# Performance work log

Hardware: AMD Instinct MI355X
Metric: run time of the kernel (lower is better)

The kernel has to match this reference:

```python
import jax, jax.numpy as jnp
import numpy as np

DIM = 1024
HEADS = 16
HD = DIM // HEADS          # 64
HID = 4 * DIM              # 4096
TPF = 1374                 # tokens_per_frame
LR = 0.1
NS_ITERS = 5
TTT_STEPS = 2
B, S = 2, 4
SN = S * TPF               # 5496


def _newton_schulz(G, iters=NS_ITERS):
    """Muon Newton-Schulz orthogonalization (quintic iteration)."""
    a, b, c = 3.4445, -4.7750, 2.0315
    X = G / (jnp.linalg.norm(G) + 1e-7)
    transposed = G.shape[0] > G.shape[1]
    if transposed:
        X = X.T
    for _ in range(iters):
        A = X @ X.T                      # [m,m], m = min(rows, cols)
        X = a * X + (b * A + c * (A @ A)) @ X
    return X.T if transposed else X


def _muon_update(p, g):
    return p - LR * _newton_schulz(g)


def setup_inputs() -> dict:
    key = jax.random.key(0)
    ks = jax.random.split(key, 8)
    inp = {
        "x": jax.random.normal(ks[0], (B, SN, DIM), jnp.float32),
        "qkv_w": jax.random.normal(ks[1], (DIM, 3 * DIM), jnp.float32) * (DIM ** -0.5),
        "qkv_b": jnp.zeros((3 * DIM,), jnp.float32),
        "qn_scale": jnp.ones((HD,), jnp.float32),
        "qn_bias": jnp.zeros((HD,), jnp.float32),
        "kn_scale": jnp.ones((HD,), jnp.float32),
        "kn_bias": jnp.zeros((HD,), jnp.float32),
        # theta: lecun-normal scale (std = 1/sqrt(fan_in))
        "ttt_gate": jax.random.normal(ks[2], (DIM, HID), jnp.float32) * (DIM ** -0.5),
        "ttt_val": jax.random.normal(ks[3], (DIM, HID), jnp.float32) * (DIM ** -0.5),
        "ttt_proj": jax.random.normal(ks[4], (HID, DIM), jnp.float32) * (HID ** -0.5),
        "proj_w": jax.random.normal(ks[5], (DIM, DIM), jnp.float32) * (DIM ** -0.5),
        "proj_b": jnp.zeros((DIM,), jnp.float32),
    }
    return inp


def reference(x, qkv_w, qkv_b, qn_scale, qn_bias, kn_scale, kn_bias,
              ttt_gate, ttt_val, ttt_proj, proj_w, proj_b):
    Bx, SNx, _ = x.shape
    qkv = x @ qkv_w + qkv_b                       # [B, SN, 3*DIM]
    q, k, v = jnp.split(qkv, 3, axis=-1)
    q = q.reshape(Bx, SNx, HEADS, HD)
    k = k.reshape(Bx, SNx, HEADS, HD)
    # per-head L2 normalize then affine NormLayer (x*scale + bias)
    q = q / (jnp.linalg.norm(q, axis=-1, keepdims=True) + 1e-6) * qn_scale + qn_bias
    k = k / (jnp.linalg.norm(k, axis=-1, keepdims=True) + 1e-6) * kn_scale + kn_bias
    q_ttt = q.reshape(-1, DIM)                    # [B*SN, DIM]
    k_ttt = k.reshape(-1, DIM)
    # no short_conv param at init -> v_mixed is identity, so v_target == v
    v_ttt = v.reshape(-1, DIM)

    theta = {"gate": ttt_gate, "val": ttt_val, "proj": ttt_proj}

    def loss_fn(p):
        h = jax.nn.swish(k_ttt @ p["gate"]) * (k_ttt @ p["val"])   # [B*SN, HID]
        pred = h @ p["proj"]                                        # [B*SN, DIM]
        return jnp.mean((pred - v_ttt) ** 2)

    for _ in range(TTT_STEPS):
        grads = jax.grad(loss_fn)(theta)
        theta = {kk: _muon_update(theta[kk], grads[kk]) for kk in theta}

    h_q = jax.nn.swish(q_ttt @ theta["gate"]) * (q_ttt @ theta["val"])
    o = (h_q @ theta["proj"]) @ proj_w + proj_b
    return o.reshape(Bx, SNx, DIM)
```

## Files before the change

### kernel.cpp

```cpp
#include <hip/hip_runtime.h>
#include <stdint.h>

#define NTOK 10992
#define NTOKA 11264
#define PMi 4194304

typedef unsigned short u16;
typedef __attribute__((ext_vector_type(8))) __bf16 b8;
typedef __attribute__((ext_vector_type(4))) float f32x4;

__device__ __forceinline__ u16 f2b(float f) {
  union { float f; uint32_t u; } v; v.f = f;
  return (u16)((v.u + 0x7fffu + ((v.u >> 16) & 1u)) >> 16);
}
__device__ __forceinline__ float b2f(u16 b) {
  union { uint32_t u; float f; } v; v.u = ((uint32_t)b) << 16; return v.f;
}
__device__ __forceinline__ uint2 pk4(u16 a, u16 b, u16 c, u16 d) {
  uint2 r; r.x = (uint32_t)a | ((uint32_t)b << 16); r.y = (uint32_t)c | ((uint32_t)d << 16);
  return r;
}
__device__ __forceinline__ void gload16(const u16* g, u16* l) {
  __builtin_amdgcn_global_load_lds((const __attribute__((address_space(1))) void*)(const void*)g,
                                   (__attribute__((address_space(3))) void*)(void*)l, 16, 0, 0);
}

struct GA {
  const u16* A[3]; const u16* B[3];
  void* C[3]; u16* O1[3]; u16* OT[3];
  const void* E0[3]; const u16* E1[3];
  int lda[3], ldb[3];
  int M, N, K, ldc, ldo1, ldt, lde0, lde1;
  float p0, p1;
};

template <int EPI, int SPLIT>
__global__ __launch_bounds__(256, 2) void gemm_bt(GA g) {
  __shared__ u16 As[128 * 32];
  __shared__ u16 Bs[128 * 32];
  int bz = blockIdx.z, koff = 0, klen = g.K;
  if constexpr (SPLIT) { koff = (bz & 1) * (g.K >> 1); bz >>= 1; klen = g.K >> 1; }
  const u16* __restrict__ A = g.A[bz] + koff;
  const u16* __restrict__ B = g.B[bz] + koff;
  const int lda = g.lda[bz], ldb = g.ldb[bz];
  const int m0 = blockIdx.y * 128, n0 = blockIdx.x * 128;
  const int tid = threadIdx.x, w = tid >> 6, lane = tid & 63;
  const int wr = (w >> 1) * 64, wc = (w & 1) * 64;
  const int ln = lane & 15, lq = lane >> 4;

  f32x4 acc[4][4];
#pragma unroll
  for (int i = 0; i < 4; ++i)
#pragma unroll
    for (int j = 0; j < 4; ++j)
#pragma unroll
      for (int r = 0; r < 4; ++r) acc[i][j][r] = 0.f;

  const u16* Ag = A + (size_t)(m0 + 32 * w + (lane >> 2)) * lda + (lane & 3) * 8;
  const u16* Bg = B + (size_t)(n0 + 32 * w + (lane >> 2)) * ldb + (lane & 3) * 8;
  u16* AsW = &As[w * 1024];
  u16* BsW = &Bs[w * 1024];
  const int nkt = klen >> 5;

  for (int kt = 0; kt < nkt; ++kt) {
    __syncthreads();
    gload16(Ag, AsW);
    gload16(Ag + (size_t)16 * lda, AsW + 512);
    gload16(Bg, BsW);
    gload16(Bg + (size_t)16 * ldb, BsW + 512);
    Ag += 32; Bg += 32;
    __syncthreads();
    b8 af[4], bfr[4];
#pragma unroll
    for (int i = 0; i < 4; ++i) af[i] = *(const b8*)&As[(wr + i * 16 + ln) * 32 + lq * 8];
#pragma unroll
    for (int j = 0; j < 4; ++j) bfr[j] = *(const b8*)&Bs[(wc + j * 16 + ln) * 32 + lq * 8];
#pragma unroll
    for (int i = 0; i < 4; ++i)
#pragma unroll
      for (int j = 0; j < 4; ++j)
        acc[i][j] = __builtin_amdgcn_mfma_f32_16x16x32_bf16(af[i], bfr[j], acc[i][j], 0, 0, 0);
  }

  float* Cf = (float*)g.C[bz];
  u16* Cb = (u16*)g.C[bz];
  u16* O1 = g.O1[bz];
  const float* E0f = (const float*)g.E0[bz];
  const u16* E0b = (const u16*)g.E0[bz];
  const u16* E1b = g.E1[bz];

#pragma unroll
  for (int i = 0; i < 4; ++i) {
    const int mb = m0 + wr + i * 16 + lq * 4;
    if (mb >= g.M) continue;
#pragma unroll
    for (int j = 0; j < 4; ++j) {
      const int n = n0 + wc + j * 16 + ln;
      if (n >= g.N) continue;
      float vv[4];
#pragma unroll
      for (int r = 0; r < 4; ++r) vv[r] = acc[i][j][r];
      if constexpr (EPI == 0) {
#pragma unroll
        for (int r = 0; r < 4; ++r) Cb[(size_t)(mb + r) * g.ldc + n] = f2b(vv[r]);
      } else if constexpr (EPI == 1) {
        const float bias = E0f[n];
#pragma unroll
        for (int r = 0; r < 4; ++r) Cb[(size_t)(mb + r) * g.ldc + n] = f2b(vv[r] + bias);
      } else if constexpr (EPI == 5) {
        u16 cq[4], oq[4];
#pragma unroll
        for (int r = 0; r < 4; ++r) {
          const int m = mb + r;
          const float f1 = b2f(E0b[(size_t)m * g.lde0 + n]);
          const float f2 = b2f(E1b[(size_t)m * g.lde1 + n]);
          cq[r] = f2b(vv[r] * f1);
          oq[r] = f2b(vv[r] * f2);
        }
        *(uint2*)&Cb[(size_t)n * g.ldt + mb] = pk4(cq[0], cq[1], cq[2], cq[3]);
        *(uint2*)&O1[(size_t)n * g.ldt + mb] = pk4(oq[0], oq[1], oq[2], oq[3]);
      } else if constexpr (EPI == 6) {
        const float bias = E0f[n];
#pragma unroll
        for (int r = 0; r < 4; ++r) Cf[(size_t)(mb + r) * g.ldc + n] = vv[r] + bias;
      } else if constexpr (EPI == 8) {
#pragma unroll
        for (int r = 0; r < 4; ++r) atomicAdd(&Cf[(size_t)(mb + r) * g.ldc + n], vv[r]);
      } else if constexpr (EPI == 16) {
        uint2 old = *(const uint2*)&Cb[(size_t)n * 1024 + mb];
        u16 nq[4];
        nq[0] = f2b(b2f((u16)(old.x & 0xffff)) - 0.1f * vv[0]);
        nq[1] = f2b(b2f((u16)(old.x >> 16)) - 0.1f * vv[1]);
        nq[2] = f2b(b2f((u16)(old.y & 0xffff)) - 0.1f * vv[2]);
        nq[3] = f2b(b2f((u16)(old.y >> 16)) - 0.1f * vv[3]);
        *(uint2*)&Cb[(size_t)n * 1024 + mb] = pk4(nq[0], nq[1], nq[2], nq[3]);
        if (O1) {
#pragma unroll
          for (int r = 0; r < 4; ++r) O1[(size_t)(mb + r) * 4096 + n] = nq[r];
        }
      }
    }
  }
}

__global__ __launch_bounds__(256, 2) void gemm_qkv(GA g) {
  __shared__ u16 As[128 * 32];
  __shared__ u16 Bs[128 * 32];
  const u16* __restrict__ A = g.A[0];
  const u16* __restrict__ B = g.B[0];
  const int lda = g.lda[0], ldb = g.ldb[0];
  const int m0 = blockIdx.y * 128, n0 = blockIdx.x * 128;
  const int tid = threadIdx.x, w = tid >> 6, lane = tid & 63;
  const int wr = (w >> 1) * 64, wc = (w & 1) * 64;
  const int ln = lane & 15, lq = lane >> 4;

  f32x4 acc[4][4];
#pragma unroll
  for (int i = 0; i < 4; ++i)
#pragma unroll
    for (int j = 0; j < 4; ++j)
#pragma unroll
      for (int r = 0; r < 4; ++r) acc[i][j][r] = 0.f;

  const u16* Ag = A + (size_t)(m0 + 32 * w + (lane >> 2)) * lda + (lane & 3) * 8;
  const u16* Bg = B + (size_t)(n0 + 32 * w + (lane >> 2)) * ldb + (lane & 3) * 8;
  u16* AsW = &As[w * 1024];
  u16* BsW = &Bs[w * 1024];
  const int nkt = g.K >> 5;

  for (int kt = 0; kt < nkt; ++kt) {
    __syncthreads();
    gload16(Ag, AsW);
    gload16(Ag + (size_t)16 * lda, AsW + 512);
    gload16(Bg, BsW);
    gload16(Bg + (size_t)16 * ldb, BsW + 512);
    Ag += 32; Bg += 32;
    __syncthreads();
    b8 af[4], bfr[4];
#pragma unroll
    for (int i = 0; i < 4; ++i) af[i] = *(const b8*)&As[(wr + i * 16 + ln) * 32 + lq * 8];
#pragma unroll
    for (int j = 0; j < 4; ++j) bfr[j] = *(const b8*)&Bs[(wc + j * 16 + ln) * 32 + lq * 8];
#pragma unroll
    for (int i = 0; i < 4; ++i)
#pragma unroll
      for (int j = 0; j < 4; ++j)
        acc[i][j] = __builtin_amdgcn_mfma_f32_16x16x32_bf16(af[i], bfr[j], acc[i][j], 0, 0, 0);
  }

  u16* qbp = (u16*)g.C[0];
  u16* kbp = g.O1[0];
  u16* kTp = g.OT[0];
  u16* vTp = g.OT[1];
  const float* bias = (const float*)g.E0[0];
  const float* qS = (const float*)g.E0[1];
  const float* kS = (const float*)g.E0[2];
  const float* qB = (const float*)g.E1[0];
  const float* kB = (const float*)g.E1[1];
  const int seg = (n0 + wc) >> 10;

#pragma unroll
  for (int i = 0; i < 4; ++i) {
    const int mb = m0 + wr + i * 16 + lq * 4;
    if (mb >= g.M) continue;
    float vb4[4][4];
// ... 378 lines not shown
#pragma unroll
        for (int r = 0; r < 4; ++r) acc[i][j][r] = 0.f;
    const u16* Ag = A + (size_t)(m0 + 32 * w + (lane >> 2)) * lda + (lane & 3) * 8;
    const u16* Bg = B + (size_t)(n0 + 32 * w + (lane >> 2)) * ldb + (lane & 3) * 8;
    u16* AsW = &As[w * 1024];
    u16* BsW = &Bs[w * 1024];
    const int nkt = gdh.K >> 5;
    for (int kt = 0; kt < nkt; ++kt) {
      __syncthreads();
      gload16(Ag, AsW);
      gload16(Ag + (size_t)16 * lda, AsW + 512);
      gload16(Bg, BsW);
      gload16(Bg + (size_t)16 * ldb, BsW + 512);
      Ag += 32; Bg += 32;
      __syncthreads();
      b8 af[4], bfr[4];
#pragma unroll
      for (int i = 0; i < 4; ++i) af[i] = *(const b8*)&As[(wr + i * 16 + ln) * 32 + lq * 8];
#pragma unroll
      for (int j = 0; j < 4; ++j) bfr[j] = *(const b8*)&Bs[(wc + j * 16 + ln) * 32 + lq * 8];
#pragma unroll
      for (int i = 0; i < 4; ++i)
#pragma unroll
        for (int j = 0; j < 4; ++j)
          acc[i][j] = __builtin_amdgcn_mfma_f32_16x16x32_bf16(af[i], bfr[j], acc[i][j], 0, 0, 0);
    }
    u16* Cb = (u16*)gdh.C[0];
    u16* O1 = gdh.O1[0];
    const u16* E0b = (const u16*)gdh.E0[0];
    const u16* E1b = gdh.E1[0];
#pragma unroll
    for (int i = 0; i < 4; ++i) {
      const int mb = m0 + wr + i * 16 + lq * 4;
      if (mb >= gdh.M) continue;
#pragma unroll
      for (int j = 0; j < 4; ++j) {
        const int n = n0 + wc + j * 16 + ln;
        u16 cq[4], oq[4];
#pragma unroll
        for (int r = 0; r < 4; ++r) {
          const int m = mb + r;
          const float f1 = b2f(E0b[(size_t)m * gdh.lde0 + n]);
          const float f2 = b2f(E1b[(size_t)m * gdh.lde1 + n]);
          cq[r] = f2b(acc[i][j][r] * f1);
          oq[r] = f2b(acc[i][j][r] * f2);
        }
        *(uint2*)&Cb[(size_t)n * gdh.ldt + mb] = pk4(cq[0], cq[1], cq[2], cq[3]);
        *(uint2*)&O1[(size_t)n * gdh.ldt + mb] = pk4(oq[0], oq[1], oq[2], oq[3]);
      }
    }
  }
}

__global__ __launch_bounds__(256, 2) void fused_gd(GA ggr, GA gdp, int nGr, int dpx) {
  __shared__ u16 As[128 * 32];
  __shared__ u16 Bs[128 * 32];
  const int tid = threadIdx.x, w = tid >> 6, lane = tid & 63;
  const int ln = lane & 15, lq = lane >> 4;
  const int bid = blockIdx.x;

  if (bid < nGr) {
    const int wr = (w >> 1) * 64, wc = (w & 1) * 64;
    const int n0 = (bid & 31) * 128;
    const int rest = bid >> 5;
    const int m0 = (rest & 7) * 128;
    int bz = rest >> 3;
    const int koff = (bz & 1) * (ggr.K >> 1); bz >>= 1;
    const int klen = ggr.K >> 1;
    const u16* __restrict__ A = ggr.A[bz] + koff;
    const u16* __restrict__ B = ggr.B[bz] + koff;
    const int lda = ggr.lda[bz], ldb = ggr.ldb[bz];
    f32x4 acc[4][4];
#pragma unroll
    for (int i = 0; i < 4; ++i)
#pragma unroll
      for (int j = 0; j < 4; ++j)
#pragma unroll
        for (int r = 0; r < 4; ++r) acc[i][j][r] = 0.f;
    const u16* Ag = A + (size_t)(m0 + 32 * w + (lane >> 2)) * lda + (lane & 3) * 8;
    const u16* Bg = B + (size_t)(n0 + 32 * w + (lane >> 2)) * ldb + (lane & 3) * 8;
    u16* AsW = &As[w * 1024];
    u16* BsW = &Bs[w * 1024];
    const int nkt = klen >> 5;
    for (int kt = 0; kt < nkt; ++kt) {
      __syncthreads();
      gload16(Ag, AsW);
      gload16(Ag + (size_t)16 * lda, AsW + 512);
      gload16(Bg, BsW);
      gload16(Bg + (size_t)16 * ldb, BsW + 512);
      Ag += 32; Bg += 32;
      __syncthreads();
      b8 af[4], bfr[4];
#pragma unroll
      for (int i = 0; i < 4; ++i) af[i] = *(const b8*)&As[(wr + i * 16 + ln) * 32 + lq * 8];
#pragma unroll
      for (int j = 0; j < 4; ++j) bfr[j] = *(const b8*)&Bs[(wc + j * 16 + ln) * 32 + lq * 8];
#pragma unroll
      for (int i = 0; i < 4; ++i)
#pragma unroll
        for (int j = 0; j < 4; ++j)
          acc[i][j] = __builtin_amdgcn_mfma_f32_16x16x32_bf16(af[i], bfr[j], acc[i][j], 0, 0, 0);
    }
    float* Cf = (float*)ggr.C[bz];
#pragma unroll
    for (int i = 0; i < 4; ++i) {
      const int mb = m0 + wr + i * 16 + lq * 4;
#pragma unroll
      for (int j = 0; j < 4; ++j) {
        const int n = n0 + wc + j * 16 + ln;
#pragma unroll
        for (int r = 0; r < 4; ++r) atomicAdd(&Cf[(size_t)(mb + r) * ggr.ldc + n], acc[i][j][r]);
      }
    }
  } else {
    const int wr = (w >> 1) * 32, wc = (w & 1) * 32;
    const int l = bid - nGr;
    const int n0 = (l % dpx) * 64;
    const int m0 = (l / dpx) * 64;
    const u16* __restrict__ A = gdp.A[0];
    const u16* __restrict__ B = gdp.B[0];
    const int lda = gdp.lda[0], ldb = gdp.ldb[0];
    f32x4 acc[2][2];
#pragma unroll
    for (int i = 0; i < 2; ++i)
#pragma unroll
      for (int j = 0; j < 2; ++j)
#pragma unroll
        for (int r = 0; r < 4; ++r) acc[i][j][r] = 0.f;
    const u16* Ag = A + (size_t)(m0 + 16 * w + (lane >> 2)) * lda + (lane & 3) * 8;
    const u16* Bg = B + (size_t)(n0 + 16 * w + (lane >> 2)) * ldb + (lane & 3) * 8;
    u16* AsW = &As[w * 512];
    u16* BsW = &Bs[w * 512];
    const int nkt = gdp.K >> 5;
    for (int kt = 0; kt < nkt; ++kt) {
      __syncthreads();
      gload16(Ag, AsW);
      gload16(Bg, BsW);
      Ag += 32; Bg += 32;
      __syncthreads();
      b8 af[2], bfr[2];
#pragma unroll
      for (int i = 0; i < 2; ++i) af[i] = *(const b8*)&As[(wr + i * 16 + ln) * 32 + lq * 8];
#pragma unroll
      for (int j = 0; j < 2; ++j) bfr[j] = *(const b8*)&Bs[(wc + j * 16 + ln) * 32 + lq * 8];
#pragma unroll
      for (int i = 0; i < 2; ++i)
#pragma unroll
        for (int j = 0; j < 2; ++j)
          acc[i][j] = __builtin_amdgcn_mfma_f32_16x16x32_bf16(af[i], bfr[j], acc[i][j], 0, 0, 0);
    }
    u16* Cb = (u16*)gdp.C[0];
    u16* OT = gdp.OT[0];
    const u16* E0b = (const u16*)gdp.E0[0];
#pragma unroll
    for (int i = 0; i < 2; ++i) {
      const int mb = m0 + wr + i * 16 + lq * 4;
#pragma unroll
      for (int j = 0; j < 2; ++j) {
        const int n = n0 + wc + j * 16 + ln;
        if (n >= gdp.N) continue;
        u16 cq[4];
#pragma unroll
        for (int r = 0; r < 4; ++r) {
          const int m = mb + r;
// ... 147 lines not shown
    }
  } else {
    const int m0 = ((int)blockIdx.y - ysplit) * 128, n0 = blockIdx.x * 128;
    const u16* __restrict__ A = gp.A[0];
    const u16* __restrict__ B = gp.B[0];
    const int lda = gp.lda[0], ldb = gp.ldb[0];
    f32x4 acc[4][4];
#pragma unroll
    for (int i = 0; i < 4; ++i)
#pragma unroll
      for (int j = 0; j < 4; ++j)
#pragma unroll
        for (int r = 0; r < 4; ++r) acc[i][j][r] = 0.f;
    const u16* Ag = A + (size_t)(m0 + 32 * w + (lane >> 2)) * lda + (lane & 3) * 8;
    const u16* Bg = B + (size_t)(n0 + 32 * w + (lane >> 2)) * ldb + (lane & 3) * 8;
    u16* AsW = &As[w * 1024];
    u16* BsW = &Bs[w * 1024];
    const int nkt = gp.K >> 5;
    for (int kt = 0; kt < nkt; ++kt) {
      __syncthreads();
      gload16(Ag, AsW);
      gload16(Ag + (size_t)16 * lda, AsW + 512);
      gload16(Bg, BsW);
      gload16(Bg + (size_t)16 * ldb, BsW + 512);
      Ag += 32; Bg += 32;
      __syncthreads();
      b8 af[4], bfr[4];
#pragma unroll
      for (int i = 0; i < 4; ++i) af[i] = *(const b8*)&As[(wr + i * 16 + ln) * 32 + lq * 8];
#pragma unroll
      for (int j = 0; j < 4; ++j) bfr[j] = *(const b8*)&Bs[(wc + j * 16 + ln) * 32 + lq * 8];
#pragma unroll
      for (int i = 0; i < 4; ++i)
#pragma unroll
        for (int j = 0; j < 4; ++j)
          acc[i][j] = __builtin_amdgcn_mfma_f32_16x16x32_bf16(af[i], bfr[j], acc[i][j], 0, 0, 0);
    }
    u16* Cb = (u16*)gp.C[0];
#pragma unroll
    for (int i = 0; i < 4; ++i) {
      const int mb = m0 + wr + i * 16 + lq * 4;
#pragma unroll
      for (int j = 0; j < 4; ++j) {
        const int n = n0 + wc + j * 16 + ln;
#pragma unroll
        for (int r = 0; r < 4; ++r) Cb[(size_t)(mb + r) * gp.ldc + n] = f2b(acc[i][j][r]);
      }
    }
  }
}

template <int EPI>
__global__ __launch_bounds__(256, 2) void gemm64(GA g) {
  if constexpr (EPI == 10 || EPI == 11 || EPI == 12) {
    if (blockIdx.x > blockIdx.y) return;
  }
  __shared__ u16 As[64 * 32];
  __shared__ u16 Bs[64 * 32];
  const int bz = blockIdx.z;
  const u16* __restrict__ A = g.A[bz];
  const u16* __restrict__ B = g.B[bz];
  const int lda = g.lda[bz], ldb = g.ldb[bz];
  const int m0 = blockIdx.y * 64, n0 = blockIdx.x * 64;
  const int tid = threadIdx.x, w = tid >> 6, lane = tid & 63;
  const int wr = (w >> 1) * 32, wc = (w & 1) * 32;
  const int ln = lane & 15, lq = lane >> 4;

  f32x4 acc[2][2];
#pragma unroll
  for (int i = 0; i < 2; ++i)
#pragma unroll
    for (int j = 0; j < 2; ++j)
#pragma unroll
      for (int r = 0; r < 4; ++r) acc[i][j][r] = 0.f;

  const u16* Ag = A + (size_t)(m0 + 16 * w + (lane >> 2)) * lda + (lane & 3) * 8;
  const u16* Bg = B + (size_t)(n0 + 16 * w + (lane >> 2)) * ldb + (lane & 3) * 8;
  u16* AsW = &As[w * 512];
  u16* BsW = &Bs[w * 512];
  const int nkt = g.K >> 5;

  for (int kt = 0; kt < nkt; ++kt) {
    __syncthreads();
    gload16(Ag, AsW);
    gload16(Bg, BsW);
    Ag += 32; Bg += 32;
    __syncthreads();
    b8 af[2], bfr[2];
#pragma unroll
    for (int i = 0; i < 2; ++i) af[i] = *(const b8*)&As[(wr + i * 16 + ln) * 32 + lq * 8];
#pragma unroll
    for (int j = 0; j < 2; ++j) bfr[j] = *(const b8*)&Bs[(wc + j * 16 + ln) * 32 + lq * 8];
#pragma unroll
    for (int i = 0; i < 2; ++i)
#pragma unroll
      for (int j = 0; j < 2; ++j)
        acc[i][j] = __builtin_amdgcn_mfma_f32_16x16x32_bf16(af[i], bfr[j], acc[i][j], 0, 0, 0);
  }

  u16* Cb = (u16*)g.C[bz];
  u16* OT = g.OT[bz];
  const u16* E0b = (const u16*)g.E0[bz];
  const u16* E1b = g.E1[bz];
  const bool offdiag = (blockIdx.x != blockIdx.y);

#pragma unroll
  for (int i = 0; i < 2; ++i) {
// ... 2 lines not shown
#pragma unroll
    for (int j = 0; j < 2; ++j) {
      const int n = n0 + wc + j * 16 + ln;
      if (n >= g.N) continue;
      float vv[4];
#pragma unroll
      for (int r = 0; r < 4; ++r) vv[r] = acc[i][j][r];
      if constexpr (EPI == 0) {
#pragma unroll
        for (int r = 0; r < 4; ++r) Cb[(size_t)(mb + r) * g.ldc + n] = f2b(vv[r]);
      } else if constexpr (EPI == 2) {
        u16 cq[4];
#pragma unroll
        for (int r = 0; r < 4; ++r) {
          const int m = mb + r;
          const u16 ub = f2b((vv[r] - b2f(E0b[(size_t)m * g.lde0 + n])) * g.p0);
          Cb[(size_t)m * g.ldc + n] = ub;
          cq[r] = ub;
        }
        *(uint2*)&OT[(size_t)n * g.ldt + mb] = pk4(cq[0], cq[1], cq[2], cq[3]);
      } else if constexpr (EPI == 10) {
        u16 cq[4];
#pragma unroll
        for (int r = 0; r < 4; ++r) {
          cq[r] = f2b(vv[r]);
          Cb[(size_t)(mb + r) * g.ldc + n] = cq[r];
        }
        if (offdiag)
          *(uint2*)&Cb[(size_t)n * g.ldc + mb] = pk4(cq[0], cq[1], cq[2], cq[3]);
      } else if constexpr (EPI == 11) {
        u16 cq[4];
#pragma unroll
        for (int r = 0; r < 4; ++r) {
          cq[r] = f2b(g.p0 * b2f(E0b[(size_t)(mb + r) * g.lde0 + n]) + g.p1 * vv[r]);
          Cb[(size_t)(mb + r) * g.ldc + n] = cq[r];
        }
        if (offdiag)
          *(uint2*)&Cb[(size_t)n * g.ldc + mb] = pk4(cq[0], cq[1], cq[2], cq[3]);
      } else if constexpr (EPI == 12) {
        const uint2 t2u = *(const uint2*)&E1b[(size_t)n * g.lde1 + mb];
        const float t2v[4] = { b2f((u16)(t2u.x & 0xffff)), b2f((u16)(t2u.x >> 16)),
                               b2f((u16)(t2u.y & 0xffff)), b2f((u16)(t2u.y >> 16)) };
        u16 cq[4];
#pragma unroll
        for (int r = 0; r < 4; ++r) {
          const int m = mb + r;
          const float t1 = b2f(E1b[(size_t)m * g.lde1 + n]);
          const float a0 = b2f(E0b[(size_t)m * g.lde0 + n]);
          cq[r] = f2b(g.p0 * a0 + g.p1 * (t1 + t2v[r]) + vv[r]);
          Cb[(size_t)m * g.ldc + n] = cq[r];
        }
        if (offdiag)
          *(uint2*)&Cb[(size_t)n * g.ldc + mb] = pk4(cq[0], cq[1], cq[2], cq[3]);
      } else if constexpr (EPI == 15) {
        const uint2 eu = *(const uint2*)&E0b[(size_t)n * g.lde0 + mb];
        const float e4[4] = { b2f((u16)(eu.x & 0xffff)), b2f((u16)(eu.x >> 16)),
                              b2f((u16)(eu.y & 0xffff)), b2f((u16)(eu.y >> 16)) };
#pragma unroll
        for (int r = 0; r < 4; ++r)
          Cb[(size_t)(mb + r) * g.ldc + n] = f2b(g.p0 * e4[r] + vv[r]);
      }
    }
  }
}

__global__ __launch_bounds__(256) void tr_f32b(const float* __restrict__ in, u16* __restrict__ out,
                                               int Cin, int Rtot) {
  __shared__ u16 t[32][33];
  const int c0 = blockIdx.x * 32, r0 = blockIdx.y * 32;
  const int tx = threadIdx.x, ty = threadIdx.y;
#pragma unroll
  for (int yy = 0; yy < 4; ++yy) {
    const int rr = ty * 4 + yy;
    t[rr][tx] = f2b(in[(size_t)(r0 + rr) * Cin + c0 + tx]);
  }
  __syncthreads();
#pragma unroll
  for (int yy = 0; yy < 4; ++yy) {
    const int cc = ty * 4 + yy;
    out[(size_t)(c0 + cc) * Rtot + r0 + tx] = t[tx][cc];
  }
}

__global__ void cvt_k(const float* __restrict__ in, u16* __restrict__ out, int n) {
  const int i = blockIdx.x * 256 + threadIdx.x;
  if (i < n) out[i] = f2b(in[i]);
}

__global__ void diag_k(float* __restrict__ out, int n, float val) {
  const int i = blockIdx.x * 256 + threadIdx.x;
  if (i < n) out[i] = val;
}

__global__ void addI_k(const u16* __restrict__ W, u16* __restrict__ M, float a) {
  const int i = blockIdx.x * 256 + threadIdx.x;
  const size_t o = (size_t)blockIdx.y * 1048576;
  u16 v = W[o + i];
  if ((i >> 10) == (i & 1023)) v = f2b(a + b2f(v));
  M[o + i] = v;
}

__global__ __launch_bounds__(256) void sumsq_k(const float* __restrict__ g, float* __restrict__ out) {
  const int b = blockIdx.y;
  const float* p = g + (size_t)b * PMi;
  float s = 0.f;
  for (int i = blockIdx.x * 256 + threadIdx.x; i < PMi; i += gridDim.x * 256) {
    float v = p[i]; s += v * v;
  }
  for (int off = 32; off > 0; off >>= 1) s += __shfl_xor(s, off);
  __shared__ float red[4];
  if ((threadIdx.x & 63) == 0) red[threadIdx.x >> 6] = s;
  __syncthreads();
  if (threadIdx.x == 0) atomicAdd(out + b, red[0] + red[1] + red[2] + red[3]);
}

__global__ __launch_bounds__(256) void scale_tr(const float* __restrict__ g, const float* __restrict__ ss,
                                                u16* __restrict__ Xb, u16* __restrict__ XbT) {
  const int b = blockIdx.z;
  __shared__ u16 t[32][33];
  const float r = 1.f / (sqrtf(ss[b]) + 1e-7f);
  const float* G = g + (size_t)b * PMi;
  u16* X = Xb + (size_t)b * PMi;
  u16* XT = XbT + (size_t)b * PMi;
  const int j0 = blockIdx.x * 32, i0 = blockIdx.y * 32;
  const int tx = threadIdx.x, ty = threadIdx.y;
#pragma unroll
  for (int yy = 0; yy < 4; ++yy) {
    const int rr = ty * 4 + yy;
    const u16 v = f2b(G[(size_t)(i0 + rr) * 4096 + j0 + tx] * r);
    X[(size_t)(i0 + rr) * 4096 + j0 + tx] = v;
    t[rr][tx] = v;
  }
  __syncthreads();
#pragma unroll
  for (int yy = 0; yy < 4; ++yy) {
    const int cc = ty * 4 + yy;
    XT[(size_t)(j0 + cc) * 1024 + i0 + tx] = t[tx][cc];
  }
}

static GA mk(const u16* A, const u16* B, void* C, int M, int N, int K,
             int lda, int ldb, int ldc) {
  GA a{};
  a.A[0] = a.A[1] = a.A[2] = A;
  a.B[0] = a.B[1] = a.B[2] = B;
  a.C[0] = a.C[1] = a.C[2] = C;
  a.lda[0] = a.lda[1] = a.lda[2] = lda;
  a.ldb[0] = a.ldb[1] = a.ldb[2] = ldb;
  a.M = M; a.N = N; a.K = K; a.ldc = ldc;
  return a;
}

extern "C" void kernel_launch(void* const* d_in, const int* in_sizes, int n_in,
                              void* d_out, int out_size, void* d_ws, size_t ws_size,
                              hipStream_t stream) {
  (void)in_sizes; (void)n_in;
  const float* x      = (const float*)d_in[0];
  const float* qkv_w  = (const float*)d_in[1];
  const float* qkv_b  = (const float*)d_in[2];
  const float* qn_s   = (const float*)d_in[3];
  const float* qn_b   = (const float*)d_in[4];
  const float* kn_s   = (const float*)d_in[5];
  const float* kn_b   = (const float*)d_in[6];
  const float* g_gate = (const float*)d_in[7];
  const float* g_val  = (const float*)d_in[8];
  const float* g_proj = (const float*)d_in[9];
  const float* proj_w = (const float*)d_in[10];
  const float* proj_b = (const float*)d_in[11];
  float* out = (float*)d_out;

  const size_t PM = PMi;
  const size_t TD = (size_t)NTOKA * 1024;
  const size_t PERS = 127926528ull;

  auto needD = [&](int chk) {
    return PERS + 9ull * (size_t)chk * 8192 + 4ull * (size_t)chk * 2048 + 50331648ull + 8192;
  };
  auto needP = [&](int chk) {
    return PERS + 7ull * (size_t)chk * 8192 + 2ull * (size_t)chk * 2048 + 50331648ull + 8192;
  };
  auto needU = [&](int chk) {
    return PERS + 5ull * (size_t)chk * 8192 + 2ull * (size_t)chk * 2048 + 50331648ull + 4096;
  };
  int CHKr, MODE;
  if      (ws_size >= needD(5632)) { CHKr = 5632; MODE = 2; }
  else if (ws_size >= needD(4096)) { CHKr = 4096; MODE = 2; }
  else if (ws_size >= needP(5632)) { CHKr = 5632; MODE = 1; }
  else if (ws_size >= needU(5632)) { CHKr = 5632; MODE = 0; }
  else if (ws_size >= needP(2816)) { CHKr = 2816; MODE = 1; }
  else if (ws_size >= needP(2048)) { CHKr = 2048; MODE = 1; }
  else if (ws_size >= needU(1408)) { CHKr = 1408; MODE = 0; }
  else {
    diag_k<<<dim3((out_size + 255) / 256), dim3(256), 0, stream>>>(out, out_size,
                                                                   (float)(ws_size >> 20));
    return;
  }

  char* p = (char*)d_ws;
  auto carve = [&](size_t bytes) { char* r = p; p += (bytes + 255) & ~(size_t)255; return (void*)r; };
  auto cdiv = [](int a, int b) { return (a + b - 1) / b; };

  u16* Gt     = (u16*)carve(PM * 2);
  u16* Vt     = (u16*)carve(PM * 2);
  u16* Pt     = (u16*)carve(PM * 2);
  u16* Pb     = (u16*)carve(PM * 2);
  u16* projWt = (u16*)carve(1048576ull * 2);
  u16* qb     = (u16*)carve(TD * 2);
  u16* kb     = (u16*)carve(TD * 2);
  u16* vT     = (u16*)carve(TD * 2);
  u16* kT     = (u16*)carve(TD * 2);
  float* ssq  = (float*)carve(256);
  char* arena = p;

  u16* xb    = (u16*)arena;
  u16* qkvWt = (u16*)(arena + 23068672);
  const size_t CB = (size_t)CHKr * 4096 * 2;
  const size_t DP = (size_t)CHKr * 1024 * 2;
  u16 *f1A[2], *f2A[2], *hhA[2], *hTA[2], *dpTA[2], *dpBA[2], *dzvT;
  float* gAll;
  if (MODE == 2) {
    f1A[0] = (u16*)(arena + 0 * CB);  f2A[0] = (u16*)(arena + 1 * CB);
    hhA[0] = (u16*)(arena + 2 * CB);  hTA[0] = (u16*)(arena + 3 * CB);
    f1A[1] = (u16*)(arena + 4 * CB);  f2A[1] = (u16*)(arena + 5 * CB);
    hhA[1] = (u16*)(arena + 6 * CB);  hTA[1] = (u16*)(arena + 7 * CB);
    dzvT   = (u16*)(arena + 8 * CB);
    dpTA[0] = (u16*)(arena + 9 * CB);          dpBA[0] = (u16*)(arena + 9 * CB + DP);
    dpTA[1] = (u16*)(arena + 9 * CB + 2 * DP); dpBA[1] = (u16*)(arena + 9 * CB + 3 * DP);
    gAll = (float*)(arena + 9 * CB + 4 * DP);
  } else {
    f1A[0] = f1A[1] = (u16*)arena;
    f2A[0] = f2A[1] = (u16*)(arena + CB);
    hhA[0] = (u16*)(arena + 2 * CB);
    hTA[0] = (u16*)(arena + 3 * CB);
    dzvT   = (u16*)(arena + 4 * CB);
    dpTA[0] = dpTA[1] = (u16*)(arena + 5 * CB);
    dpBA[0] = dpBA[1] = (u16*)(arena + 5 * CB + DP);
    gAll = (float*)(arena + 5 * CB + 2 * DP);
    hhA[1] = (MODE == 1) ? (u16*)(arena + 5 * CB + 2 * DP + 3 * PM * 4) : hhA[0];
    hTA[1] = (MODE == 1) ? (u16*)(arena + 6 * CB + 2 * DP + 3 * PM * 4) : hTA[0];
  }
  u16* XAb  = (u16*)arena;
  u16* XAbT = (u16*)(arena + 25165824);
  u16* Ab   = (u16*)(arena + 50331648);
  u16* Wb   = (u16*)(arena + 56623104);
  u16* Tb   = (u16*)(arena + 62914560);
  u16* Mb0  = (u16*)(arena + 69206016);
  u16* Mb1  = (u16*)(arena + 75497472);
  u16* hbuf = (u16*)arena;
  u16* PWt  = (u16*)(arena + 92274688);

  const dim3 blk(256), tb32(32, 8);
  const float inv2 = 2.0f / (10992.0f * 1024.0f);
  const float nsa = 3.4445f, nsb = -4.7750f, nsc = 2.0315f;

  hipMemsetAsync(kT, 0, TD * 2, stream);
  hipMemsetAsync(vT, 0, TD * 2, stream);
  cvt_k<<<dim3(43968), blk, 0, stream>>>(x, xb, NTOK * 1024);
  cvt_k<<<dim3(16384), blk, 0, stream>>>(g_proj, Pb, (int)PM);
  tr_f32b<<<dim3(96, 32), tb32, 0, stream>>>(qkv_w, qkvWt, 3072, 1024);
  tr_f32b<<<dim3(32, 32), tb32, 0, stream>>>(proj_w, projWt, 1024, 1024);
  tr_f32b<<<dim3(128, 32), tb32, 0, stream>>>(g_gate, Gt, 4096, 1024);
  tr_f32b<<<dim3(128, 32), tb32, 0, stream>>>(g_val, Vt, 4096, 1024);
  tr_f32b<<<dim3(32, 128), tb32, 0, stream>>>(g_proj, Pt, 1024, 4096);

  {
    GA a = mk(xb, qkvWt, qb, NTOK, 3072, 1024, 1024, 1024, 1024);
    a.O1[0] = kb; a.OT[0] = kT; a.OT[1] = vT;
    a.E0[0] = qkv_b; a.E0[1] = qn_s; a.E0[2] = kn_s;
    a.E1[0] = (const u16*)qn_b; a.E1[1] = (const u16*)kn_b;
    gemm_qkv<<<dim3(24, 86, 1), blk, 0, stream>>>(a);
  }

  for (int step = 0; step < 2; ++step) {
    hipMemsetAsync(gAll, 0, 3 * PM * 4, stream);
    if (MODE == 2) {
      const int NC = cdiv(NTOK, CHKr);
      int c0P = 0, vcP = 0, mtP = 0;
      for (int ci = 0; ci < NC; ++ci) {
        const int c0 = ci * CHKr;
        const int vc = (NTOK - c0 < CHKr) ? (NTOK - c0) : CHKr;
        const int mt = cdiv(vc, 128);
        const int par = ci & 1, parP = par ^ 1;
        const int tail = (ci == NC - 1 && vc < CHKr);
        if (tail) hipMemsetAsync(hTA[par], 0, CB, stream);
        GA agv{};
        agv.A[0] = kb + (size_t)c0 * 1024; agv.lda[0] = 1024;
        agv.B[0] = Gt; agv.B[1] = Vt; agv.ldb[0] = 1024;
        agv.C[0] = f1A[par]; agv.O1[0] = f2A[par]; agv.O1[1] = hhA[par]; agv.OT[0] = hTA[par];
        agv.M = vc; agv.N = 4096; agv.K = 1024; agv.ldc = 4096; agv.ldt = CHKr;
        if (ci == 0) {
          gemm_gv<0><<<dim3(32, mt, 1), blk, 0, stream>>>(agv);
        } else {
          GA adh{};
          adh.A[0] = dpBA[parP]; adh.B[0] = Pb; adh.lda[0] = 1024; adh.ldb[0] = 1024;
          adh.C[0] = hhA[parP]; adh.O1[0] = dzvT;
          adh.E0[0] = f1A[parP]; adh.E1[0] = f2A[parP];
          adh.M = vcP; adh.N = 4096; adh.K = 1024; adh.ldt = CHKr;
          adh.lde0 = 4096; adh.lde1 = 4096;
          fused_hg<<<dim3(32, mt + mtP, 1), blk, 0, stream>>>(adh, agv, mt);
        }
        if (tail) hipMemsetAsync(dpTA[par], 0, DP, stream);
        GA adp = mk(Pt, hhA[par], dpTA[par], 1024, vc, 4096, 4096, 4096, CHKr);
        adp.OT[0] = dpBA[par]; adp.ldt = 1024;
        adp.E0[0] = vT + c0; adp.lde0 = NTOKA; adp.p0 = inv2;
        const int dpx = cdiv(vc, 64);
        if (ci == 0) {
          gemm64<2><<<dim3(dpx, 16, 1), blk, 0, stream>>>(adp);
        } else {
          GA agr{};
          agr.A[0] = kT + c0P; agr.A[1] = kT + c0P; agr.A[2] = dpTA[parP];
          agr.lda[0] = NTOKA; agr.lda[1] = NTOKA; agr.lda[2] = CHKr;
          agr.B[0] = hhA[parP]; agr.B[1] = dzvT; agr.B[2] = hTA[parP];
          agr.ldb[0] = agr.ldb[1] = agr.ldb[2] = CHKr;
          agr.C[0] = gAll; agr.C[1] = gAll + PM; agr.C[2] = gAll + 2 * PM;
          agr.M = 1024; agr.N = 4096; agr.K = CHKr; agr.ldc = 4096;
          fused_gd<<<dim3(1536 + dpx * 16, 1, 1), blk, 0, stream>>>(agr, adp, 1536, dpx);
        }
        c0P = c0; vcP = vc; mtP = mt;
      }
      const int par = (NC - 1) & 1;
      if (vcP < CHKr) {
        hipMemsetAsync(hhA[par], 0, CB, stream);
        hipMemsetAsync(dzvT, 0, CB, stream);
      }
      {
        GA adh = mk(dpBA[par], Pb, hhA[par], vcP, 4096, 1024, 1024, 1024, 0);
        adh.O1[0] = dzvT; adh.ldt = CHKr;
        adh.E0[0] = f1A[par]; adh.lde0 = 4096; adh.E1[0] = f2A[par]; adh.lde1 = 4096;
        gemm_bt<5, 0><<<dim3(32, mtP, 1), blk, 0, stream>>>(adh);
      }
      {
        GA agr{};
        agr.A[0] = kT + c0P; agr.A[1] = kT + c0P; agr.A[2] = dpTA[par];
        agr.lda[0] = NTOKA; agr.lda[1] = NTOKA; agr.lda[2] = CHKr;
        agr.B[0] = hhA[par]; agr.B[1] = dzvT; agr.B[2] = hTA[par];
        agr.ldb[0] = agr.ldb[1] = agr.ldb[2] = CHKr;
        agr.C[0] = gAll; agr.C[1] = gAll + PM; agr.C[2] = gAll + 2 * PM;
        agr.M = 1024; agr.N = 4096; agr.K = CHKr; agr.ldc = 4096;
        gemm_bt<8, 1><<<dim3(32, 8, 6), blk, 0, stream>>>(agr);
      }
    } else {
      int havePend = 0;
      GA pendGA{};
      for (int ci = 0, c0 = 0; c0 < NTOK; ++ci, c0 += CHKr) {
        const int vc = (NTOK - c0 < CHKr) ? (NTOK - c0) : CHKr;
        const int mt = cdiv(vc, 128);
        const u16* kc = kb + (size_t)c0 * 1024;
        u16* hhp = hhA[ci & 1];
        u16* hTp = hTA[ci & 1];
        if (vc < CHKr) hipMemsetAsync(hTp, 0, CB, stream);
        {
          GA agv{};
          agv.A[0] = kc; agv.lda[0] = 1024;
          agv.B[0] = Gt; agv.B[1] = Vt; agv.ldb[0] = 1024;
          agv.C[0] = f1A[0]; agv.O1[0] = f2A[0]; agv.O1[1] = hhp; agv.OT[0] = hTp;
          agv.M = vc; agv.N = 4096; agv.K = 1024; agv.ldc = 4096; agv.ldt = CHKr;
          if (MODE == 1 && havePend) {
            fused_gg<<<dim3(32, mt + 48, 1), blk, 0, stream>>>(pendGA, agv, mt);
            havePend = 0;
          } else {
            gemm_gv<0><<<dim3(32, mt, 1), blk, 0, stream>>>(agv);
          }
        }
        if (vc < CHKr) {
          hipMemsetAsync(dzvT, 0, CB, stream);
          hipMemsetAsync(dpTA[0], 0, DP, stream);
        }
        {
          GA a = mk(Pt, hhp, dpTA[0], 1024, vc, 4096, 4096, 4096, CHKr);
          a.OT[0] = dpBA[0]; a.ldt = 1024;
          a.E0[0] = vT + c0; a.lde0 = NTOKA; a.p0 = inv2;
          gemm64<2><<<dim3(cdiv(vc, 64), 16, 1), blk, 0, stream>>>(a);
        }
        if (vc < CHKr) hipMemsetAsync(hhp, 0, CB, stream);
        {
          GA a = mk(dpBA[0], Pb, hhp, vc, 4096, 1024, 1024, 1024, 0);
          a.O1[0] = dzvT; a.ldt = CHKr;
          a.E0[0] = f1A[0]; a.lde0 = 4096; a.E1[0] = f2A[0]; a.lde1 = 4096;
          gemm_bt<5, 0><<<dim3(32, mt, 1), blk, 0, stream>>>(a);
        }
        {
          GA a{};
          a.A[0] = kT + c0; a.A[1] = kT + c0; a.A[2] = dpTA[0];
          a.lda[0] = NTOKA; a.lda[1] = NTOKA; a.lda[2] = CHKr;
          a.B[0] = hhp; a.B[1] = dzvT; a.B[2] = hTp;
          a.ldb[0] = a.ldb[1] = a.ldb[2] = CHKr;
          a.C[0] = gAll; a.C[1] = gAll + PM; a.C[2] = gAll + 2 * PM;
          a.M = 1024; a.N = 4096; a.K = CHKr; a.ldc = 4096;
          const int last = (c0 + CHKr >= NTOK);
          if (MODE == 1 && !last) { pendGA = a; havePend = 1; }
          else gemm_bt<8, 1><<<dim3(32, 8, 6), blk, 0, stream>>>(a);
        }
      }
    }
    hipMemsetAsync(ssq, 0, 16, stream);
    sumsq_k<<<dim3(512, 3), blk, 0, stream>>>(gAll, ssq);
    scale_tr<<<dim3(128, 32, 3), tb32, 0, stream>>>(gAll, ssq, XAb, XAbT);

    {
      GA a{};
      for (int b = 0; b < 3; ++b) {
        a.A[b] = XAb + (size_t)b * PM; a.B[b] = XAb + (size_t)b * PM;
        a.C[b] = Ab + (size_t)b * 1048576;
        a.lda[b] = 4096; a.ldb[b] = 4096;
      }
      a.M = 1024; a.N = 1024; a.K = 4096; a.ldc = 1024;
      gemm64<10><<<dim3(16, 16, 3), blk, 0, stream>>>(a);
    }
    for (int it = 0; it < 5; ++it) {
      {
        GA a{};
        for (int b = 0; b < 3; ++b) {
          a.A[b] = Ab + (size_t)b * 1048576; a.B[b] = Ab + (size_t)b * 1048576;
          a.C[b] = Wb + (size_t)b * 1048576; a.E0[b] = Ab + (size_t)b * 1048576;
          a.lda[b] = 1024; a.ldb[b] = 1024;
        }
        a.M = 1024; a.N = 1024; a.K = 1024; a.ldc = 1024; a.lde0 = 1024;
        a.p0 = nsb; a.p1 = nsc;
        gemm64<11><<<dim3(16, 16, 3), blk, 0, stream>>>(a);
      }
      if (it == 0) {
        addI_k<<<dim3(4096, 3), blk, 0, stream>>>(Wb, Mb0, nsa);
        {
          GA a{};
          for (int b = 0; b < 3; ++b) {
            a.A[b] = Wb + (size_t)b * 1048576; a.B[b] = Ab + (size_t)b * 1048576;
            a.C[b] = Tb + (size_t)b * 1048576;
            a.lda[b] = 1024; a.ldb[b] = 1024;
          }
          a.M = 1024; a.N = 1024; a.K = 1024; a.ldc = 1024;
          gemm64<0><<<dim3(16, 16, 3), blk, 0, stream>>>(a);
        }
      } else if (it < 4) {
        u16* Mti = (it & 1) ? Mb0 : Mb1;
        u16* Mto = (it & 1) ? Mb1 : Mb0;
        GA gt{}, gm{};
        for (int b = 0; b < 3; ++b) {
          gt.A[b] = Wb + (size_t)b * 1048576; gt.B[b] = Ab + (size_t)b * 1048576;
          gt.C[b] = Tb + (size_t)b * 1048576;
          gt.lda[b] = 1024; gt.ldb[b] = 1024;
          gm.A[b] = Mti + (size_t)b * 1048576; gm.B[b] = Wb + (size_t)b * 1048576;
          gm.C[b] = Mto + (size_t)b * 1048576; gm.E0[b] = Mti + (size_t)b * 1048576;
          gm.lda[b] = 1024; gm.ldb[b] = 1024;
        }
        gt.M = gt.N = 1024; gt.K = 1024; gt.ldc = 1024;
        gm.M = gm.N = 1024; gm.K = 1024; gm.ldc = 1024; gm.lde0 = 1024; gm.p0 = nsa;
        fused_mt<<<dim3(16, 32, 3), blk, 0, stream>>>(gt, gm);
      } else {
        GA a{};
        for (int b = 0; b < 3; ++b) {
          a.A[b] = Wb + (size_t)b * 1048576; a.B[b] = Mb1 + (size_t)b * 1048576;
          a.C[b] = Mb0 + (size_t)b * 1048576; a.E0[b] = Mb1 + (size_t)b * 1048576;
          a.lda[b] = 1024; a.ldb[b] = 1024;
        }
        a.M = 1024; a.N = 1024; a.K = 1024; a.ldc = 1024; a.lde0 = 1024; a.p0 = nsa;
        gemm64<15><<<dim3(16, 16, 3), blk, 0, stream>>>(a);
      }
      if (it < 4) {
        GA a{};
        for (int b = 0; b < 3; ++b) {
          a.A[b] = Tb + (size_t)b * 1048576; a.B[b] = Wb + (size_t)b * 1048576;
          a.C[b] = Ab + (size_t)b * 1048576;
          a.E0[b] = Ab + (size_t)b * 1048576; a.E1[b] = Tb + (size_t)b * 1048576;
          a.lda[b] = 1024; a.ldb[b] = 1024;
        }
        a.M = 1024; a.N = 1024; a.K = 1024; a.ldc = 1024;
        a.lde0 = 1024; a.lde1 = 1024;
        a.p0 = nsa * nsa; a.p1 = nsa;
        gemm64<12><<<dim3(16, 16, 3), blk, 0, stream>>>(a);
      }
    }
    {
      GA a{};
      for (int b = 0; b < 3; ++b) {
        a.A[b] = Mb0 + (size_t)b * 1048576; a.B[b] = XAbT + (size_t)b * PM;
// ... 25 lines not shown
```

Measured before the change: 5.569 ms.

## Fuse setup transposes into QKV GEMM, drop memsets and addI kernel

Folds the weight conversions and transposes (gate, val, proj, proj_w and the bf16 copy of proj) into extra blocks of the QKV GEMM launch, so they share one kernel. It replaces the full-buffer memsets of kT/vT with a tail-zeroing kernel and fuses the Newton-Schulz identity add into a new GEMM epilogue. The gradient GEMM drops split-K in MODE 2, with the first chunk storing instead of atomically adding, which removes the gAll memset. It also clips the final chunk's K to skip padding. These changes cut launch count and memory traffic, but they rely on the tail zeroing and the first-chunk store covering every element that was previously cleared.

Result: no change. 5.648 ms (+1.4%).

```diff
diff --git a/kernel.cpp b/kernel.cpp
--- a/kernel.cpp
+++ b/kernel.cpp
@@ -32,6 +32,11 @@
   int lda[3], ldb[3];
   int M, N, K, ldc, ldo1, ldt, lde0, lde1;
   float p0, p1;
+};
+
+struct SP {
+  const float *gg, *gv, *gp, *pw;
+  u16 *Gt, *Vt, *Pt, *projWt, *Pb;
 };
 
 template <int EPI, int SPLIT>
@@ -103,10 +108,6 @@
       if constexpr (EPI == 0) {
 #pragma unroll
         for (int r = 0; r < 4; ++r) Cb[(size_t)(mb + r) * g.ldc + n] = f2b(vv[r]);
-      } else if constexpr (EPI == 1) {
-        const float bias = E0f[n];
-#pragma unroll
-        for (int r = 0; r < 4; ++r) Cb[(size_t)(mb + r) * g.ldc + n] = f2b(vv[r] + bias);
       } else if constexpr (EPI == 5) {
         u16 cq[4], oq[4];
 #pragma unroll
@@ -143,14 +144,47 @@
   }
 }
 
-__global__ __launch_bounds__(256, 2) void gemm_qkv(GA g) {
+__global__ __launch_bounds__(256, 2) void setup_fused(GA g, SP s) {
   __shared__ u16 As[128 * 32];
   __shared__ u16 Bs[128 * 32];
+  const int tid = threadIdx.x;
+
+  if ((int)blockIdx.y >= 86) {
+    const int id = ((int)blockIdx.y - 86) * 24 + (int)blockIdx.x;
+    if (id >= 14336) return;
+    if (id >= 13312) {
+      const int off = (id - 13312) * 4096;
+#pragma unroll 4
+      for (int i = tid; i < 4096; i += 256) s.Pb[off + i] = f2b(s.gp[off + i]);
+      return;
+    }
+    const float* in; u16* outp; int Cin, Rtot, bx, by;
+    if (id < 4096)       { in = s.gg; outp = s.Gt; Cin = 4096; Rtot = 1024; bx = id & 127; by = id >> 7; }
+    else if (id < 8192)  { const int t2 = id - 4096; in = s.gv; outp = s.Vt; Cin = 4096; Rtot = 1024; bx = t2 & 127; by = t2 >> 7; }
+    else if (id < 12288) { const int t2 = id - 8192; in = s.gp; outp = s.Pt; Cin = 1024; Rtot = 4096; bx = t2 & 31; by = t2 >> 5; }
+    else                 { const int t2 = id - 12288; in = s.pw; outp = s.projWt; Cin = 1024; Rtot = 1024; bx = t2 & 31; by = t2 >> 5; }
+    const int c0 = bx * 32, r0 = by * 32;
+    const int tx = tid & 31, ty = tid >> 5;
+    u16 (*tt)[33] = (u16(*)[33])As;
+#pragma unroll
+    for (int yy = 0; yy < 4; ++yy) {
+      const int rr = ty * 4 + yy;
+      tt[rr][tx] = f2b(in[(size_t)(r0 + rr) * Cin + c0 + tx]);
+    }
+    __syncthreads();
+#pragma unroll
+    for (int yy = 0; yy < 4; ++yy) {
+      const int cc = ty * 4 + yy;
+      outp[(size_t)(c0 + cc) * Rtot + r0 + tx] = tt[tx][cc];
+    }
+    return;
+  }
+
   const u16* __restrict__ A = g.A[0];
   const u16* __restrict__ B = g.B[0];
   const int lda = g.lda[0], ldb = g.ldb[0];
   const int m0 = blockIdx.y * 128, n0 = blockIdx.x * 128;
-  const int tid = threadIdx.x, w = tid >> 6, lane = tid & 63;
+  const int w = tid >> 6, lane = tid & 63;
   const int wr = (w >> 1) * 64, wc = (w & 1) * 64;
   const int ln = lane & 15, lq = lane >> 4;
 
@@ -635,6 +669,7 @@
   }
 }
 
+template <int FIRST>
 __global__ __launch_bounds__(256, 2) void fused_gd(GA ggr, GA gdp, int nGr, int dpx) {
   __shared__ u16 As[128 * 32];
   __shared__ u16 Bs[128 * 32];
@@ -647,11 +682,9 @@
     const int n0 = (bid & 31) * 128;
     const int rest = bid >> 5;
     const int m0 = (rest & 7) * 128;
-    int bz = rest >> 3;
-    const int koff = (bz & 1) * (ggr.K >> 1); bz >>= 1;
-    const int klen = ggr.K >> 1;
-    const u16* __restrict__ A = ggr.A[bz] + koff;
-    const u16* __restrict__ B = ggr.B[bz] + koff;
+    const int bz = rest >> 3;
+    const u16* __restrict__ A = ggr.A[bz];
+    const u16* __restrict__ B = ggr.B[bz];
     const int lda = ggr.lda[bz], ldb = ggr.ldb[bz];
     f32x4 acc[4][4];
 #pragma unroll
@@ -664,7 +697,7 @@
     const u16* Bg = B + (size_t)(n0 + 32 * w + (lane >> 2)) * ldb + (lane & 3) * 8;
     u16* AsW = &As[w * 1024];
     u16* BsW = &Bs[w * 1024];
-    const int nkt = klen >> 5;
+    const int nkt = ggr.K >> 5;
     for (int kt = 0; kt < nkt; ++kt) {
       __syncthreads();
       gload16(Ag, AsW);
@@ -692,7 +725,10 @@
       for (int j = 0; j < 4; ++j) {
         const int n = n0 + wc + j * 16 + ln;
 #pragma unroll
-        for (int r = 0; r < 4; ++r) atomicAdd(&Cf[(size_t)(mb + r) * ggr.ldc + n], acc[i][j][r]);
+        for (int r = 0; r < 4; ++r) {
+          if constexpr (FIRST) Cf[(size_t)(mb + r) * ggr.ldc + n] = acc[i][j][r];
+          else atomicAdd(&Cf[(size_t)(mb + r) * ggr.ldc + n], acc[i][j][r]);
+        }
       }
     }
   } else {
@@ -946,7 +982,7 @@
 
 template <int EPI>
 __global__ __launch_bounds__(256, 2) void gemm64(GA g) {
-  if constexpr (EPI == 10 || EPI == 11 || EPI == 12) {
+  if constexpr (EPI == 10 || EPI == 11 || EPI == 12 || EPI == 13) {
     if (blockIdx.x > blockIdx.y) return;
   }
   __shared__ u16 As[64 * 32];
@@ -1055,6 +1091,22 @@
         }
         if (offdiag)
           *(uint2*)&Cb[(size_t)n * g.ldc + mb] = pk4(cq[0], cq[1], cq[2], cq[3]);
+      } else if constexpr (EPI == 13) {
+        u16 cq[4], mq[4];
+#pragma unroll
+        for (int r = 0; r < 4; ++r) {
+          const int m = mb + r;
+          cq[r] = f2b(g.p0 * b2f(E0b[(size_t)m * g.lde0 + n]) + g.p1 * vv[r]);
+          Cb[(size_t)m * g.ldc + n] = cq[r];
+          float wv = b2f(cq[r]);
+          if (m == n) wv += 3.4445f;
+          mq[r] = f2b(wv);
+          OT[(size_t)m * 1024 + n] = mq[r];
+        }
+        if (offdiag) {
+          *(uint2*)&Cb[(size_t)n * g.ldc + mb] = pk4(cq[0], cq[1], cq[2], cq[3]);
+          *(uint2*)&OT[(size_t)n * 1024 + mb] = pk4(mq[0], mq[1], mq[2], mq[3]);
+        }
       } else if constexpr (EPI == 15) {
         const uint2 eu = *(const uint2*)&E0b[(size_t)n * g.lde0 + mb];
         const float e4[4] = { b2f((u16)(eu.x & 0xffff)), b2f((u16)(eu.x >> 16)),
@@ -1095,12 +1147,10 @@
   if (i < n) out[i] = val;
 }
 
-__global__ void addI_k(const u16* __restrict__ W, u16* __restrict__ M, float a) {
-  const int i = blockIdx.x * 256 + threadIdx.x;
-  const size_t o = (size_t)blockIdx.y * 1048576;
-  u16 v = W[o + i];
-  if ((i >> 10) == (i & 1023)) v = f2b(a + b2f(v));
-  M[o + i] = v;
+__global__ void zero_tail(u16* a, u16* b) {
+  u16* p = (blockIdx.y ? b : a) + (size_t)blockIdx.x * NTOKA + NTOK;
+  p[threadIdx.x & 255] = 0;
+  if (threadIdx.x < 16) p[256 + threadIdx.x] = 0;
 }
 
 __global__ __launch_bounds__(256) void sumsq_k(const float* __restrict__ g, float* __restrict__ out) {
@@ -1202,6 +1252,7 @@
   char* p = (char*)d_ws;
   auto carve = [&](size_t bytes) { char* r = p; p += (bytes + 255) & ~(size_t)255; return (void*)r; };
   auto cdiv = [](int a, int b) { return (a + b - 1) / b; };
+  auto mini = [](int a, int b) { return a < b ? a : b; };
 
   u16* Gt     = (u16*)carve(PM * 2);
   u16* Vt     = (u16*)carve(PM * 2);
@@ -1256,26 +1307,20 @@
   const float inv2 = 2.0f / (10992.0f * 1024.0f);
   const float nsa = 3.4445f, nsb = -4.7750f, nsc = 2.0315f;
 
-  hipMemsetAsync(kT, 0, TD * 2, stream);
-  hipMemsetAsync(vT, 0, TD * 2, stream);
+  zero_tail<<<dim3(1024, 2), blk, 0, stream>>>(kT, vT);
   cvt_k<<<dim3(43968), blk, 0, stream>>>(x, xb, NTOK * 1024);
-  cvt_k<<<dim3(16384), blk, 0, stream>>>(g_proj, Pb, (int)PM);
   tr_f32b<<<dim3(96, 32), tb32, 0, stream>>>(qkv_w, qkvWt, 3072, 1024);
-  tr_f32b<<<dim3(32, 32), tb32, 0, stream>>>(proj_w, projWt, 1024, 1024);
-  tr_f32b<<<dim3(128, 32), tb32, 0, stream>>>(g_gate, Gt, 4096, 1024);
-  tr_f32b<<<dim3(128, 32), tb32, 0, stream>>>(g_val, Vt, 4096, 1024);
-  tr_f32b<<<dim3(32, 128), tb32, 0, stream>>>(g_proj, Pt, 1024, 4096);
-
   {
     GA a = mk(xb, qkvWt, qb, NTOK, 3072, 1024, 1024, 1024, 1024);
     a.O1[0] = kb; a.OT[0] = kT; a.OT[1] = vT;
     a.E0[0] = qkv_b; a.E0[1] = qn_s; a.E0[2] = kn_s;
     a.E1[0] = (const u16*)qn_b; a.E1[1] = (const u16*)kn_b;
-    gemm_qkv<<<dim3(24, 86, 1), blk, 0, stream>>>(a);
+    SP s{g_gate, g_val, g_proj, proj_w, Gt, Vt, Pt, projWt, Pb};
+    setup_fused<<<dim3(24, 684, 1), blk, 0, stream>>>(a, s);
   }
 
   for (int step = 0; step < 2; ++step) {
-    hipMemsetAsync(gAll, 0, 3 * PM * 4, stream);
+    if (MODE != 2) hipMemsetAsync(gAll, 0, 3 * PM * 4, stream);
     if (MODE == 2) {
       const int NC = cdiv(NTOK, CHKr);
       int c0P = 0, vcP = 0, mtP = 0;
@@ -1317,7 +1362,10 @@
           agr.ldb[0] = agr.ldb[1] = agr.ldb[2] = CHKr;
           agr.C[0] = gAll; agr.C[1] = gAll + PM; agr.C[2] = gAll + 2 * PM;
           agr.M = 1024; agr.N = 4096; agr.K = CHKr; agr.ldc = 4096;
-          fused_gd<<<dim3(1536 + dpx * 16, 1, 1), blk, 0, stream>>>(agr, adp, 1536, dpx);
+          if (ci == 1)
+            fused_gd<1><<<dim3(768 + dpx * 16, 1, 1), blk, 0, stream>>>(agr, adp, 768, dpx);
+          else
+            fused_gd<0><<<dim3(768 + dpx * 16, 1, 1), blk, 0, stream>>>(agr, adp, 768, dpx);
         }
         c0P = c0; vcP = vc; mtP = mt;
       }
@@ -1339,7 +1387,7 @@
         agr.B[0] = hhA[par]; agr.B[1] = dzvT; agr.B[2] = hTA[par];
         agr.ldb[0] = agr.ldb[1] = agr.ldb[2] = CHKr;
         agr.C[0] = gAll; agr.C[1] = gAll + PM; agr.C[2] = gAll + 2 * PM;
-        agr.M = 1024; agr.N = 4096; agr.K = CHKr; agr.ldc = 4096;
+        agr.M = 1024; agr.N = 4096; agr.K = mini(CHKr, NTOKA - c0P); agr.ldc = 4096;
         gemm_bt<8, 1><<<dim3(32, 8, 6), blk, 0, stream>>>(agr);
       }
     } else {
@@ -1389,7 +1437,7 @@
           a.B[0] = hhp; a.B[1] = dzvT; a.B[2] = hTp;
           a.ldb[0] = a.ldb[1] = a.ldb[2] = CHKr;
           a.C[0] = gAll; a.C[1] = gAll + PM; a.C[2] = gAll + 2 * PM;
-          a.M = 1024; a.N = 4096; a.K = CHKr; a.ldc = 4096;
+          a.M = 1024; a.N = 4096; a.K = mini(CHKr, NTOKA - c0); a.ldc = 4096;
           const int last = (c0 + CHKr >= NTOK);
           if (MODE == 1 && !last) { pendGA = a; havePend = 1; }
           else gemm_bt<8, 1><<<dim3(32, 8, 6), blk, 0, stream>>>(a);
@@ -1416,14 +1464,15 @@
         for (int b = 0; b < 3; ++b) {
           a.A[b] = Ab + (size_t)b * 1048576; a.B[b] = Ab + (size_t)b * 1048576;
           a.C[b] = Wb + (size_t)b * 1048576; a.E0[b] = Ab + (size_t)b * 1048576;
+          a.OT[b] = Mb0 + (size_t)b * 1048576;
           a.lda[b] = 1024; a.ldb[b] = 1024;
         }
         a.M = 1024; a.N = 1024; a.K = 1024; a.ldc = 1024; a.lde0 = 1024;
         a.p0 = nsb; a.p1 = nsc;
-        gemm64<11><<<dim3(16, 16, 3), blk, 0, stream>>>(a);
+        if (it == 0) gemm64<13><<<dim3(16, 16, 3), blk, 0, stream>>>(a);
+        else gemm64<11><<<dim3(16, 16, 3), blk, 0, stream>>>(a);
       }
       if (it == 0) {
-        addI_k<<<dim3(4096, 3), blk, 0, stream>>>(Wb, Mb0, nsa);
         {
           GA a{};
           for (int b = 0; b < 3; ++b) {
```
